# Performance work log

Measured on AMD Instinct MI355X. Metric: run time of the kernel, lower is better.

Reference implementation:

```python
import jax, jax.numpy as jnp
import numpy as np

EPS = 1e-9


def _elementwise_ciou(b1, b2):
    # b1, b2: [..., 4] xyxy boxes. Direct O(N) CIoU (== diag of pairwise CIoU).
    x1a, y1a, x2a, y2a = b1[..., 0], b1[..., 1], b1[..., 2], b1[..., 3]
    x1b, y1b, x2b, y2b = b2[..., 0], b2[..., 1], b2[..., 2], b2[..., 3]

    iw = jnp.clip(jnp.minimum(x2a, x2b) - jnp.maximum(x1a, x1b), 0.0)
    ih = jnp.clip(jnp.minimum(y2a, y2b) - jnp.maximum(y1a, y1b), 0.0)
    inter = iw * ih
    area_a = (x2a - x1a) * (y2a - y1a)
    area_b = (x2b - x1b) * (y2b - y1b)
    union = area_a + area_b - inter
    iou = inter / (union + EPS)

    # enclosing box diagonal squared
    cw = jnp.maximum(x2a, x2b) - jnp.minimum(x1a, x1b)
    ch = jnp.maximum(y2a, y2b) - jnp.minimum(y1a, y1b)
    c2 = cw * cw + ch * ch + EPS

    # center distance squared
    dx = (x1b + x2b - x1a - x2a) * 0.5
    dy = (y1b + y2b - y1a - y2a) * 0.5
    rho2 = dx * dx + dy * dy

    # aspect-ratio consistency term
    wa, ha = x2a - x1a, y2a - y1a
    wb, hb = x2b - x1b, y2b - y1b
    v = (4.0 / (jnp.pi ** 2)) * jnp.square(
        jnp.arctan(wb / (hb + EPS)) - jnp.arctan(wa / (ha + EPS)))
    alpha = v / (1.0 - iou + v + EPS)
    return iou - rho2 / c2 - alpha * v


def _make_boxes(key, B, A):
    k1, k2 = jax.random.split(key)
    cxy = jax.random.uniform(k1, (B, A, 2), jnp.float32, 0.0, 1280.0)
    wh = jax.random.uniform(k2, (B, A, 2), jnp.float32, 4.0, 200.0)
    return jnp.concatenate([cxy - wh * 0.5, cxy + wh * 0.5], axis=-1)


def setup_inputs() -> dict:
    key = jax.random.key(0)
    B, A = 64, 33600
    k1, k2, k3, k4 = jax.random.split(key, 4)
    predicts_bbox = _make_boxes(k1, B, A)
    targets_bbox = _make_boxes(k2, B, A)
    valid_masks = jax.random.bernoulli(k3, 0.3, (B, A))
    box_norm = jax.random.uniform(k4, (B, A), jnp.float32) * valid_masks
    cls_norm = jnp.maximum(valid_masks.sum().astype(jnp.float32), 1.0)
    return {
        "predicts_bbox": predicts_bbox,
        "targets_bbox": targets_bbox,
        "valid_masks": valid_masks,
        "box_norm": box_norm,
        "cls_norm": cls_norm,
    }


def reference(predicts_bbox, targets_bbox, valid_masks, box_norm, cls_norm):
    m = valid_masks.astype(predicts_bbox.dtype)  # [B, A]
    iou = _elementwise_ciou(predicts_bbox, targets_bbox) * m
    loss_iou = ((1.0 - iou) * box_norm * m).sum() / cls_norm
    return loss_iou, iou
```

## Files before the change

kernel.cpp:

```cpp
#include <hip/hip_runtime.h>
#include <math.h>

#define EPSF 1e-9f
#define DEPTH 8

__device__ __forceinline__ float fast_atan(float z) {
    float az = fabsf(z);
    float rz = __builtin_amdgcn_rcpf(az);
    float t  = az > 1.0f ? rz : az;
    float t2 = t * t;
    float p = fmaf(t2, 0.0208351f, -0.0851330f);
    p = fmaf(t2, p, 0.1801410f);
    p = fmaf(t2, p, -0.3302995f);
    p = fmaf(t2, p, 0.9998660f);
    p = p * t;
    float r = az > 1.0f ? 1.5707963f - p : p;
    return z < 0.0f ? -r : r;
}

__device__ __forceinline__ float ciou_masked(float4 a, float4 b, float m,
                                             float bn, float* acc) {
    float iw = fminf(a.z, b.z) - fmaxf(a.x, b.x); iw = fmaxf(iw, 0.0f);
    float ih = fminf(a.w, b.w) - fmaxf(a.y, b.y); ih = fmaxf(ih, 0.0f);
    float inter = iw * ih;

    float wa = a.z - a.x, ha = a.w - a.y;
    float wb = b.z - b.x, hb = b.w - b.y;
    float uni = wa * ha + wb * hb - inter;
    float iou = inter * __builtin_amdgcn_rcpf(uni + EPSF);

    float cw = fmaxf(a.z, b.z) - fminf(a.x, b.x);
    float ch = fmaxf(a.w, b.w) - fminf(a.y, b.y);
    float c2 = fmaf(cw, cw, fmaf(ch, ch, EPSF));

    float dx = (b.x + b.z - a.x - a.z) * 0.5f;
    float dy = (b.y + b.w - a.y - a.w) * 0.5f;
    float rho2 = fmaf(dx, dx, dy * dy);

    float hap = ha + EPSF, hbp = hb + EPSF;
    float num = fmaf(wb, hap, -wa * hbp);
    float den = fmaf(hap, hbp, wa * wb);
    float datan = fast_atan(num * __builtin_amdgcn_rcpf(den));

    const float c4pi2 = 0.40528473456f;
    float v = c4pi2 * datan * datan;
    float av = v * v * __builtin_amdgcn_rcpf(1.0f - iou + v + EPSF);

    float ciou = iou - rho2 * __builtin_amdgcn_rcpf(c2) - av;
    float iou_m = ciou * m;
    *acc += (1.0f - iou_m) * bn * m;
    return iou_m;
}

__global__ __launch_bounds__(256, 4) void box_loss_deep(
    const float4* __restrict__ pb, const float4* __restrict__ tb,
    const int*    __restrict__ mask, const float* __restrict__ bnorm,
    float* __restrict__ iou_out, float* __restrict__ partials)
{
    const int base = blockIdx.x * (256 * DEPTH) + threadIdx.x;
    float acc = 0.0f;

    int    mk[DEPTH];
    float  bn[DEPTH];
    #pragma unroll
    for (int u = 0; u < DEPTH; ++u) {
        int i = base + u * 256;
        mk[u] = mask[i]; bn[u] = bnorm[i];
    }

    float4 a[DEPTH], b[DEPTH];
    #pragma unroll
    for (int u = 0; u < DEPTH; ++u) {
        a[u] = make_float4(0.f, 0.f, 1.f, 1.f);
        b[u] = make_float4(0.f, 0.f, 1.f, 1.f);
        int i = base + u * 256;
        if (mk[u]) { a[u] = pb[i]; b[u] = tb[i]; }
    }

    #pragma unroll
    for (int u = 0; u < DEPTH; ++u) {
        int i = base + u * 256;
        iou_out[i] = ciou_masked(a[u], b[u], (float)mk[u], bn[u], &acc);
    }

    #pragma unroll
    for (int off = 32; off > 0; off >>= 1)
        acc += __shfl_down(acc, off, 64);
    if ((threadIdx.x & 63) == 0)
        partials[blockIdx.x * 4 + (threadIdx.x >> 6)] = acc;
}

__global__ __launch_bounds__(256) void box_loss_tail(
    const float4* __restrict__ pb, const float4* __restrict__ tb,
    const int*    __restrict__ mask, const float* __restrict__ bnorm,
    float* __restrict__ iou_out, float* __restrict__ partials,
    int start, int n)
{
    const int i = start + blockIdx.x * blockDim.x + threadIdx.x;
    float acc = 0.0f;
    float r = 0.0f;
    bool ok = i < n;
    if (ok) r = ciou_masked(pb[i], tb[i], (float)mask[i], bnorm[i], &acc);
    if (ok) iou_out[i] = r;
    #pragma unroll
    for (int off = 32; off > 0; off >>= 1)
        acc += __shfl_down(acc, off, 64);
    if ((threadIdx.x & 63) == 0)
        partials[blockIdx.x * 4 + (threadIdx.x >> 6)] = acc;
}

__global__ __launch_bounds__(256) void box_loss_final(
    const float* __restrict__ partials, const float* __restrict__ cls_norm,
    float* __restrict__ out, int nparts)
{
    float acc = 0.0f;
    for (int i = threadIdx.x; i < nparts; i += 256) acc += partials[i];
    #pragma unroll
    for (int off = 32; off > 0; off >>= 1)
        acc += __shfl_down(acc, off, 64);
    __shared__ float lds[4];
    const int lane = threadIdx.x & 63;
    const int wid  = threadIdx.x >> 6;
    if (lane == 0) lds[wid] = acc;
    __syncthreads();
    if (threadIdx.x == 0)
        out[0] = (lds[0] + lds[1] + lds[2] + lds[3]) / cls_norm[0];
}

extern "C" void kernel_launch(void* const* d_in, const int* in_sizes, int n_in,
                              void* d_out, int out_size, void* d_ws, size_t ws_size,
                              hipStream_t stream) {
    const float4* pb    = (const float4*)d_in[0];
    const float4* tb    = (const float4*)d_in[1];
    const int*    mask  = (const int*)  d_in[2];
    const float*  bnorm = (const float*)d_in[3];
    const float*  cls   = (const float*)d_in[4];
    float*        out   = (float*)d_out;
    float*        part  = (float*)d_ws;
    const int n = in_sizes[2];

    const int per_block = 256 * DEPTH;
    const int full = n / per_block;
    const int rem  = n - full * per_block;

    if (full > 0)
        box_loss_deep<<<full, 256, 0, stream>>>(pb, tb, mask, bnorm,
                                                out + 1, part);
    int nparts = full * 4;
    if (rem > 0) {
        const int tg = (rem + 255) / 256;
        box_loss_tail<<<tg, 256, 0, stream>>>(pb, tb, mask, bnorm, out + 1,
                                              part + nparts, full * per_block, n);
        nparts += tg * 4;
    }
    box_loss_final<<<1, 256, 0, stream>>>(part, cls, out, nparts);
}
```

Before: 123.0 us.

## Vectorize mask/norm loads and drop mask-gated box loads

Each thread now handles four contiguous elements per chunk, so mask and box_norm are read as int4/float4 vector loads instead of scalar loads. Box loads are unconditional rather than skipped when the mask is zero, which removes divergence and the dependency on the mask load. The cost is that box data for masked-out elements (about 70%) is now fetched, raising DRAM traffic. The output stores become per-thread strided and less coalesced.

```diff
diff --git a/kernel.cpp b/kernel.cpp
--- a/kernel.cpp
+++ b/kernel.cpp
@@ -2,7 +2,8 @@
 #include <math.h>
 
 #define EPSF 1e-9f
-#define DEPTH 8
+#define CHUNK 4
+#define OUTER 2
 
 __device__ __forceinline__ float fast_atan(float z) {
     float az = fabsf(z);
@@ -57,30 +58,35 @@
     const int*    __restrict__ mask, const float* __restrict__ bnorm,
     float* __restrict__ iou_out, float* __restrict__ partials)
 {
-    const int base = blockIdx.x * (256 * DEPTH) + threadIdx.x;
-    float acc = 0.0f;
+    const int base = blockIdx.x * (256 * CHUNK * OUTER);
+    const int t    = threadIdx.x;
 
-    int    mk[DEPTH];
-    float  bn[DEPTH];
+    const int4*   mask4 = (const int4*)  (mask  + base);
+    const float4* bn4   = (const float4*)(bnorm + base);
+
+    int4   mk[OUTER];
+    float4 bv[OUTER];
+    float4 a[OUTER][CHUNK], b[OUTER][CHUNK];
+
     #pragma unroll
-    for (int u = 0; u < DEPTH; ++u) {
-        int i = base + u * 256;
-        mk[u] = mask[i]; bn[u] = bnorm[i];
+    for (int o = 0; o < OUTER; ++o) {
+        mk[o] = mask4[o * 256 + t];
+        bv[o] = bn4[o * 256 + t];
+        const int e0 = base + o * (256 * CHUNK) + t * CHUNK;
+        #pragma unroll
+        for (int k = 0; k < CHUNK; ++k) { a[o][k] = pb[e0 + k]; b[o][k] = tb[e0 + k]; }
     }
 
-    float4 a[DEPTH], b[DEPTH];
+    float acc = 0.0f;
     #pragma unroll
-    for (int u = 0; u < DEPTH; ++u) {
-        a[u] = make_float4(0.f, 0.f, 1.f, 1.f);
-        b[u] = make_float4(0.f, 0.f, 1.f, 1.f);
-        int i = base + u * 256;
-        if (mk[u]) { a[u] = pb[i]; b[u] = tb[i]; }
-    }
-
-    #pragma unroll
-    for (int u = 0; u < DEPTH; ++u) {
-        int i = base + u * 256;
-        iou_out[i] = ciou_masked(a[u], b[u], (float)mk[u], bn[u], &acc);
+    for (int o = 0; o < OUTER; ++o) {
+        const int e0 = base + o * (256 * CHUNK) + t * CHUNK;
+        const float m0 = (float)mk[o].x, m1 = (float)mk[o].y;
+        const float m2 = (float)mk[o].z, m3 = (float)mk[o].w;
+        iou_out[e0 + 0] = ciou_masked(a[o][0], b[o][0], m0, bv[o].x, &acc);
+        iou_out[e0 + 1] = ciou_masked(a[o][1], b[o][1], m1, bv[o].y, &acc);
+        iou_out[e0 + 2] = ciou_masked(a[o][2], b[o][2], m2, bv[o].z, &acc);
+        iou_out[e0 + 3] = ciou_masked(a[o][3], b[o][3], m3, bv[o].w, &acc);
     }
 
     #pragma unroll
@@ -139,7 +145,7 @@
     float*        part  = (float*)d_ws;
     const int n = in_sizes[2];
 
-    const int per_block = 256 * DEPTH;
+    const int per_block = 256 * CHUNK * OUTER;
     const int full = n / per_block;
     const int rem  = n - full * per_block;
 
```

Result: no change. 124.5 us (+1.3%).
